# Optimization experiments

Hardware: AMD Instinct MI355X
Metric: run time of the kernel (lower is better)

## Reference

```python
import jax, jax.numpy as jnp
import numpy as np

# FP4 (E2M1) code table: nibble = [sign(1) | exp(2) | mantissa(1)]
# magnitudes for codes 0..7: 0, 0.5, 1, 1.5, 2, 3, 4, 6; codes 8..15 are negated.
_MAG = np.array([0.0, 0.5, 1.0, 1.5, 2.0, 3.0, 4.0, 6.0], dtype=np.float32)
FP4_LUT = jnp.asarray(np.concatenate([_MAG, -_MAG]))  # [16]

BLOCK = 16  # scale-factor block size along in_features


def setup_inputs() -> dict:
    key = jax.random.key(0)
    k0, k1, k2, k3, k4 = jax.random.split(key, 5)
    M, K, N = 32, 8192, 8192  # tokens, in_features, out_features
    inp = jax.random.normal(k0, (M, K), dtype=jnp.float32)
    qweight = jax.random.randint(k1, (N, K // 2), 0, 256, dtype=jnp.int32)  # packed FP4 pairs
    scales = jax.random.uniform(k2, (N, K // BLOCK), dtype=jnp.float32)      # per-block scales
    amax = jax.random.uniform(k3, (1,), dtype=jnp.float32) + 0.5             # global scale
    bias = jax.random.normal(k4, (N,), dtype=jnp.float32)
    return {"input": inp, "qweight": qweight, "scales": scales, "amax": amax, "bias": bias}


def _dequantize(qweight, scales, amax):
    N = qweight.shape[0]
    low = qweight & 0xF            # first element of each pair
    high = (qweight >> 4) & 0xF    # second element
    nibbles = jnp.stack([low, high], axis=-1).reshape(N, -1)  # [N, K]
    vals = FP4_LUT[nibbles]                                   # [N, K] fp4 values
    # per-block scaling: block of BLOCK contiguous in-features shares one scale
    w = (vals.reshape(N, -1, BLOCK) * scales[..., None]).reshape(N, -1)
    return w * amax[0]


def reference(input, qweight, scales, amax, bias):
    weight = _dequantize(qweight, scales, amax)   # [N, K] full-precision weight
    return input @ weight.T + bias                # F.linear
```

## Files before the change

### kernel.cpp

```cpp
#include <hip/hip_runtime.h>
#include <hip/hip_bf16.h>

#define M_DIM 32
#define K_DIM 8192
#define N_DIM 8192
#define KS 16
#define KCH (K_DIM / KS)
#define CHK 128
#define NCHK (KCH / CHK)
#define STEPS (CHK / 32)
#define NPB 128
#define MAIN_BLOCKS ((N_DIM / NPB) * KS)

#define QW_ROWI4 (K_DIM / 8)
#define SC_ROW (K_DIM / 16)

#define QROW 17
#define AROW 136
#define SROW 9

typedef _Float16 half8   __attribute__((ext_vector_type(8)));
typedef _Float16 half4_t __attribute__((ext_vector_type(4)));
typedef float    floatx4 __attribute__((ext_vector_type(4)));

__device__ __forceinline__ uint32_t dec2(uint32_t b) {
  uint32_t c0 = b & 0xFu, c1 = (b >> 4) & 0xFu;
  uint32_t m0 = c0 & 7u, m1 = c1 & 7u;
  uint32_t t0 = min(28u * m0, m0 + 28u);
  uint32_t t1 = min(28u * m1, m1 + 28u);
  return (t0 << 9) | ((c0 & 8u) << 12)
       | (t1 << 25) | ((c1 & 8u) << 28);
}

__device__ __forceinline__ half8 decode8p(uint32_t q, _Float16 s) {
  union { uint32_t u[4]; half8 h; } w;
  w.u[0] = dec2(q & 0xFFu);
  w.u[1] = dec2((q >> 8) & 0xFFu);
  w.u[2] = dec2((q >> 16) & 0xFFu);
  w.u[3] = dec2((q >> 24) & 0xFFu);
  half8 sv = {s, s, s, s, s, s, s, s};
  return w.h * sv;
}

__global__ void convertA_kernel(const floatx4* __restrict__ in4,
                                half4_t* __restrict__ out4) {
  int idx = blockIdx.x * blockDim.x + threadIdx.x;
  floatx4 f = in4[idx];
  half4_t h;
  h[0] = (_Float16)f[0]; h[1] = (_Float16)f[1];
  h[2] = (_Float16)f[2]; h[3] = (_Float16)f[3];
  out4[idx] = h;
}

__global__ void reduce_kernel(const floatx4* __restrict__ part,
                              const floatx4* __restrict__ bias4,
                              floatx4* __restrict__ out4) {
  int idx = blockIdx.x * blockDim.x + threadIdx.x;
  floatx4 acc = bias4[idx & (N_DIM / 4 - 1)];
#pragma unroll
  for (int s = 0; s < KS; ++s)
    acc += part[(size_t)s * (M_DIM * N_DIM / 4) + idx];
  out4[idx] = acc;
}

template <bool F16A>
__global__ __launch_bounds__(256, 4) void fp4_linear_kernel(
    const void*  __restrict__ Av,
    const int4*  __restrict__ qw4,
    const float* __restrict__ scales,
    const float* __restrict__ amaxp,
    float*       __restrict__ part)
{
  __shared__ uint32_t Qs[NPB * QROW];
  __shared__ _Float16 As[M_DIM * AROW];
  __shared__ float    Ss[NPB * SROW];

  const int t    = threadIdx.x;
  const int lane = t & 63;
  const int w    = t >> 6;
  const int ks   = blockIdx.x & (KS - 1);
  const int nb   = blockIdx.x >> 4;
  const int n0   = nb * NPB;
  const int kb   = ks * KCH;
  const float amax = amaxp[0];

  const int qr = t >> 4, qc = t & 15;
  const int4* qsrc = qw4 + (size_t)(n0 + qr) * QW_ROWI4 + ks * (KCH / 8) + qc;
  const int sr = t >> 1, sh = t & 1;
  const float* ssrc = scales + (size_t)(n0 + sr) * SC_ROW + ks * (KCH / 16) + sh * 4;
  const int ar16 = t >> 4, ac16 = t & 15;
  const _Float16* asrc16 =
      (const _Float16*)Av + (size_t)ar16 * K_DIM + kb + ac16 * 8;
  const int ar32 = t >> 5, ac32 = t & 31;
  const float* asrc32 = (const float*)Av + (size_t)ar32 * K_DIM + kb + ac32 * 4;

  int4    qreg[8];
  half8   areg16[2];
  floatx4 areg32[4];
  floatx4 sreg;

  {
#pragma unroll
    for (int j = 0; j < 8; ++j)
      qreg[j] = qsrc[(size_t)j * 16 * QW_ROWI4];
    if (F16A) {
#pragma unroll
      for (int j = 0; j < 2; ++j)
        areg16[j] = *(const half8*)(asrc16 + (size_t)j * 16 * K_DIM);
    } else {
#pragma unroll
      for (int j = 0; j < 4; ++j)
        areg32[j] = *(const floatx4*)(asrc32 + (size_t)j * 8 * K_DIM);
    }
    sreg = *(const floatx4*)ssrc;
  }

  const int row  = lane & 15;
  const int quad = lane >> 4;
  const int nloc = w * 32;
  const uint32_t* qAp = &Qs[(nloc + row) * QROW];
  const uint32_t* qBp = &Qs[(nloc + 16 + row) * QROW];
  const _Float16* a0p = &As[row * AROW];
  const _Float16* a1p = &As[(row + 16) * AROW];
  const float*    sAp = &Ss[(nloc + row) * SROW];
  const float*    sBp = &Ss[(nloc + 16 + row) * SROW];

  floatx4 acc00 = {0.f, 0.f, 0.f, 0.f};
  floatx4 acc01 = {0.f, 0.f, 0.f, 0.f};
  floatx4 acc10 = {0.f, 0.f, 0.f, 0.f};
  floatx4 acc11 = {0.f, 0.f, 0.f, 0.f};

  for (int c = 0; c < NCHK; ++c) {
    if (c) __syncthreads();

#pragma unroll
    for (int j = 0; j < 8; ++j) {
      uint32_t pk = ((uint32_t)qreg[j].x & 0xFFu)
                  | (((uint32_t)qreg[j].y & 0xFFu) << 8)
                  | (((uint32_t)qreg[j].z & 0xFFu) << 16)
                  | (((uint32_t)qreg[j].w & 0xFFu) << 24);
      Qs[(j * 16 + qr) * QROW + qc] = pk;
    }
    if (F16A) {
#pragma unroll
      for (int j = 0; j < 2; ++j)
        *(half8*)&As[(j * 16 + ar16) * AROW + ac16 * 8] = areg16[j];
    } else {
#pragma unroll
      for (int j = 0; j < 4; ++j) {
        floatx4 f = areg32[j];
        half4_t h;
        h[0] = (_Float16)f[0]; h[1] = (_Float16)f[1];
        h[2] = (_Float16)f[2]; h[3] = (_Float16)f[3];
        *(half4_t*)&As[(j * 8 + ar32) * AROW + ac32 * 4] = h;
      }
    }
    {
      float* sd = &Ss[sr * SROW + sh * 4];
      sd[0] = sreg[0] * amax; sd[1] = sreg[1] * amax;
      sd[2] = sreg[2] * amax; sd[3] = sreg[3] * amax;
    }
    __syncthreads();

    if (c + 1 < NCHK) {
      const int co = c + 1;
#pragma unroll
      for (int j = 0; j < 8; ++j)
        qreg[j] = qsrc[(size_t)j * 16 * QW_ROWI4 + co * (CHK / 8)];
      if (F16A) {
#pragma unroll
        for (int j = 0; j < 2; ++j)
          areg16[j] = *(const half8*)(asrc16 + (size_t)j * 16 * K_DIM + co * CHK);
      } else {
#pragma unroll
        for (int j = 0; j < 4; ++j)
          areg32[j] = *(const floatx4*)(asrc32 + (size_t)j * 8 * K_DIM + co * CHK);
      }
      sreg = *(const floatx4*)(ssrc + co * (CHK / 16));
    }

#pragma unroll
    for (int it = 0; it < STEPS; ++it) {
      const uint32_t qA = qAp[it * 4 + quad];
      const uint32_t qB = qBp[it * 4 + quad];
      const _Float16 sA = (_Float16)sAp[it * 2 + (quad >> 1)];
      const _Float16 sB = (_Float16)sBp[it * 2 + (quad >> 1)];
      half8 bA = decode8p(qA, sA);
      half8 bB = decode8p(qB, sB);
      half8 a0 = *(const half8*)(a0p + it * 32 + quad * 8);
      half8 a1 = *(const half8*)(a1p + it * 32 + quad * 8);
      acc00 = __builtin_amdgcn_mfma_f32_16x16x32_f16(a0, bA, acc00, 0, 0, 0);
      acc01 = __builtin_amdgcn_mfma_f32_16x16x32_f16(a0, bB, acc01, 0, 0, 0);
      acc10 = __builtin_amdgcn_mfma_f32_16x16x32_f16(a1, bA, acc10, 0, 0, 0);
      acc11 = __builtin_amdgcn_mfma_f32_16x16x32_f16(a1, bB, acc11, 0, 0, 0);
    }
  }

  float* pb = part + (size_t)ks * (M_DIM * N_DIM);
#pragma unroll
  for (int r = 0; r < 4; ++r) {
    const int m = quad * 4 + r;
    float* o0 = pb + (size_t)m * N_DIM + n0 + nloc;
    float* o1 = pb + (size_t)(m + 16) * N_DIM + n0 + nloc;
    o0[row]      = acc00[r];
    o0[16 + row] = acc01[r];
    o1[row]      = acc10[r];
    o1[16 + row] = acc11[r];
  }
}

extern "C" void kernel_launch(void* const* d_in, const int* in_sizes, int n_in,
                              void* d_out, int out_size, void* d_ws, size_t ws_size,
                              hipStream_t stream) {
  const float* inp    = (const float*)d_in[0];
  const int4*  qw4    = (const int4*)d_in[1];
  const float* scales = (const float*)d_in[2];
  const float* amaxp  = (const float*)d_in[3];
  const float* bias   = (const float*)d_in[4];
  float* out = (float*)d_out;

  const size_t part_bytes = (size_t)KS * M_DIM * N_DIM * sizeof(float);
  const size_t a16_bytes  = (size_t)M_DIM * K_DIM * sizeof(_Float16);
  float* partp = (float*)d_ws;

  if (ws_size >= part_bytes + a16_bytes) {
    _Float16* Af16 = (_Float16*)((char*)d_ws + part_bytes);
    convertA_kernel<<<M_DIM * K_DIM / 4 / 256, 256, 0, stream>>>(
        (const floatx4*)inp, (half4_t*)Af16);
    fp4_linear_kernel<true><<<MAIN_BLOCKS, 256, 0, stream>>>(
        Af16, qw4, scales, amaxp, partp);
  } else {
    fp4_linear_kernel<false><<<MAIN_BLOCKS, 256, 0, stream>>>(
        inp, qw4, scales, amaxp, partp);
  }
  reduce_kernel<<<M_DIM * N_DIM / 4 / 256, 256, 0, stream>>>(
      (const floatx4*)partp, (const floatx4*)bias, (floatx4*)out);
}
```

Baseline: 219.3 us.

## Repack FP4 weights into tile-contiguous layout before the main GEMM kernel

Adds a pre-pass kernel that compresses the int32-per-byte weight array into packed bytes arranged contiguously per block tile and k-chunk. The main kernel then loads each tile with two coalesced 16-byte loads per thread and stores them with vector LDS writes, instead of eight strided int4 loads plus packing. The fallback path is rewritten to use atomic accumulation into a bias-initialised output. The repack runs on every call and reads the full weight array, so it adds an extra pass over global memory.

Result: slower. 245.8 us (+12.1%).

```diff
diff --git a/kernel.cpp b/kernel.cpp
--- a/kernel.cpp
+++ b/kernel.cpp
@@ -10,14 +10,17 @@
 #define NCHK (KCH / CHK)
 #define STEPS (CHK / 32)
 #define NPB 128
-#define MAIN_BLOCKS ((N_DIM / NPB) * KS)
+#define NBLK (N_DIM / NPB)
+#define MAIN_BLOCKS (NBLK * KS)
 
 #define QW_ROWI4 (K_DIM / 8)
 #define SC_ROW (K_DIM / 16)
 
-#define QROW 17
+#define QROW 20
 #define AROW 136
 #define SROW 9
+
+#define QP_TILE_U4 512
 
 typedef _Float16 half8   __attribute__((ext_vector_type(8)));
 typedef _Float16 half4_t __attribute__((ext_vector_type(4)));
@@ -42,6 +45,27 @@
   return w.h * sv;
 }
 
+__device__ __forceinline__ uint32_t pack4(int4 v) {
+  return ((uint32_t)v.x & 0xFFu) | (((uint32_t)v.y & 0xFFu) << 8)
+       | (((uint32_t)v.z & 0xFFu) << 16) | (((uint32_t)v.w & 0xFFu) << 24);
+}
+
+__global__ __launch_bounds__(256) void repack_kernel(
+    const int4* __restrict__ qw4, uint4* __restrict__ qp) {
+  const int g  = blockIdx.x * 256 + threadIdx.x;
+  const int u  = g & 511;
+  const int c  = (g >> 9) & 3;
+  const int ks = (g >> 11) & 15;
+  const int nb = g >> 15;
+  const int r  = u >> 2, c4 = u & 3;
+  const int4* src = qw4 + (size_t)(nb * NPB + r) * QW_ROWI4
+                  + ks * (KCH / 8) + c * (CHK / 8) + c4 * 4;
+  int4 a = src[0], b = src[1], cc = src[2], d = src[3];
+  uint4 o;
+  o.x = pack4(a); o.y = pack4(b); o.z = pack4(cc); o.w = pack4(d);
+  qp[g] = o;
+}
+
 __global__ void convertA_kernel(const floatx4* __restrict__ in4,
                                 half4_t* __restrict__ out4) {
   int idx = blockIdx.x * blockDim.x + threadIdx.x;
@@ -63,13 +87,18 @@
   out4[idx] = acc;
 }
 
-template <bool F16A>
-__global__ __launch_bounds__(256, 4) void fp4_linear_kernel(
-    const void*  __restrict__ Av,
-    const int4*  __restrict__ qw4,
-    const float* __restrict__ scales,
-    const float* __restrict__ amaxp,
-    float*       __restrict__ part)
+__global__ void init_out_kernel(floatx4* __restrict__ out4,
+                                const floatx4* __restrict__ bias4) {
+  int idx = blockIdx.x * blockDim.x + threadIdx.x;
+  out4[idx] = bias4[idx & (N_DIM / 4 - 1)];
+}
+
+__global__ __launch_bounds__(256, 4) void fp4_linear_packed(
+    const _Float16* __restrict__ Af16,
+    const uint4*    __restrict__ qp,
+    const float*    __restrict__ scales,
+    const float*    __restrict__ amaxp,
+    float*          __restrict__ part)
 {
   __shared__ uint32_t Qs[NPB * QROW];
   __shared__ _Float16 As[M_DIM * AROW];
@@ -84,36 +113,21 @@
   const int kb   = ks * KCH;
   const float amax = amaxp[0];
 
-  const int qr = t >> 4, qc = t & 15;
-  const int4* qsrc = qw4 + (size_t)(n0 + qr) * QW_ROWI4 + ks * (KCH / 8) + qc;
+  const uint4* qtile = qp + (size_t)((nb * 16 + ks) * 4) * QP_TILE_U4;
+  const int ar = t >> 4, ac = t & 15;
+  const _Float16* asrc = Af16 + (size_t)ar * K_DIM + kb + ac * 8;
   const int sr = t >> 1, sh = t & 1;
   const float* ssrc = scales + (size_t)(n0 + sr) * SC_ROW + ks * (KCH / 16) + sh * 4;
-  const int ar16 = t >> 4, ac16 = t & 15;
-  const _Float16* asrc16 =
-      (const _Float16*)Av + (size_t)ar16 * K_DIM + kb + ac16 * 8;
-  const int ar32 = t >> 5, ac32 = t & 31;
-  const float* asrc32 = (const float*)Av + (size_t)ar32 * K_DIM + kb + ac32 * 4;
-
-  int4    qreg[8];
-  half8   areg16[2];
-  floatx4 areg32[4];
+
+  uint4   qreg[2];
+  half8   areg[2];
   floatx4 sreg;
 
-  {
-#pragma unroll
-    for (int j = 0; j < 8; ++j)
-      qreg[j] = qsrc[(size_t)j * 16 * QW_ROWI4];
-    if (F16A) {
-#pragma unroll
-      for (int j = 0; j < 2; ++j)
-        areg16[j] = *(const half8*)(asrc16 + (size_t)j * 16 * K_DIM);
-    } else {
-#pragma unroll
-      for (int j = 0; j < 4; ++j)
-        areg32[j] = *(const floatx4*)(asrc32 + (size_t)j * 8 * K_DIM);
-    }
-    sreg = *(const floatx4*)ssrc;
-  }
+  qreg[0] = qtile[t];
+  qreg[1] = qtile[256 + t];
+  areg[0] = *(const half8*)asrc;
+  areg[1] = *(const half8*)(asrc + (size_t)16 * K_DIM);
+  sreg = *(const floatx4*)ssrc;
 
   const int row  = lane & 15;
   const int quad = lane >> 4;
@@ -134,26 +148,11 @@
     if (c) __syncthreads();
 
 #pragma unroll
-    for (int j = 0; j < 8; ++j) {
-      uint32_t pk = ((uint32_t)qreg[j].x & 0xFFu)
-                  | (((uint32_t)qreg[j].y & 0xFFu) << 8)
-                  | (((uint32_t)qreg[j].z & 0xFFu) << 16)
-                  | (((uint32_t)qreg[j].w & 0xFFu) << 24);
-      Qs[(j * 16 + qr) * QROW + qc] = pk;
-    }
-    if (F16A) {
-#pragma unroll
-      for (int j = 0; j < 2; ++j)
-        *(half8*)&As[(j * 16 + ar16) * AROW + ac16 * 8] = areg16[j];
-    } else {
-#pragma unroll
-      for (int j = 0; j < 4; ++j) {
-        floatx4 f = areg32[j];
-        half4_t h;
-        h[0] = (_Float16)f[0]; h[1] = (_Float16)f[1];
-        h[2] = (_Float16)f[2]; h[3] = (_Float16)f[3];
-        *(half4_t*)&As[(j * 8 + ar32) * AROW + ac32 * 4] = h;
-      }
+    for (int j = 0; j < 2; ++j) {
+      const int u = j * 256 + t;
+      const int r = u >> 2, c4 = u & 3;
+      *(uint4*)&Qs[r * QROW + c4 * 4] = qreg[j];
+      *(half8*)&As[(j * 16 + ar) * AROW + ac * 8] = areg[j];
     }
     {
       float* sd = &Ss[sr * SROW + sh * 4];
@@ -163,20 +162,12 @@
     __syncthreads();
 
     if (c + 1 < NCHK) {
-      const int co = c + 1;
-#pragma unroll
-      for (int j = 0; j < 8; ++j)
-        qreg[j] = qsrc[(size_t)j * 16 * QW_ROWI4 + co * (CHK / 8)];
-      if (F16A) {
-#pragma unroll
-        for (int j = 0; j < 2; ++j)
-          areg16[j] = *(const half8*)(asrc16 + (size_t)j * 16 * K_DIM + co * CHK);
-      } else {
-#pragma unroll
-        for (int j = 0; j < 4; ++j)
-          areg32[j] = *(const floatx4*)(asrc32 + (size_t)j * 8 * K_DIM + co * CHK);
-      }
-      sreg = *(const floatx4*)(ssrc + co * (CHK / 16));
+      const int c1 = c + 1;
+      qreg[0] = qtile[c1 * QP_TILE_U4 + t];
+      qreg[1] = qtile[c1 * QP_TILE_U4 + 256 + t];
+      areg[0] = *(const half8*)(asrc + c1 * CHK);
+      areg[1] = *(const half8*)(asrc + (size_t)16 * K_DIM + c1 * CHK);
+      sreg = *(const floatx4*)(ssrc + c1 * (CHK / 16));
     }
 
 #pragma unroll
@@ -209,6 +200,50 @@
   }
 }
 
+__global__ __launch_bounds__(256, 4) void fp4_linear_fallback(
+    const float* __restrict__ inp, const int4* __restrict__ qw4,
+    const float* __restrict__ scales, const float* __restrict__ amaxp,
+    float* __restrict__ out) {
+  const int t = threadIdx.x, lane = t & 63, w = t >> 6;
+  const int ks = blockIdx.x & (KS - 1), nb = blockIdx.x >> 4;
+  const int n0 = nb * NPB, kb = ks * KCH;
+  const float amax = amaxp[0];
+  const int row = lane & 15, quad = lane >> 4, nloc = w * 32;
+  const int nA = n0 + nloc + row, nB = nA + 16;
+  const int4* qrowA = qw4 + (size_t)nA * QW_ROWI4;
+  const int4* qrowB = qw4 + (size_t)nB * QW_ROWI4;
+  const float* srowA = scales + (size_t)nA * SC_ROW;
+  const float* srowB = scales + (size_t)nB * SC_ROW;
+  floatx4 acc00 = {0,0,0,0}, acc01 = {0,0,0,0}, acc10 = {0,0,0,0}, acc11 = {0,0,0,0};
+  for (int k0 = kb; k0 < kb + KCH; k0 += 32) {
+    const int kq = k0 + quad * 8;
+    int4 qA = qrowA[kq >> 3], qB = qrowB[kq >> 3];
+    _Float16 sA = (_Float16)(srowA[kq >> 4] * amax);
+    _Float16 sB = (_Float16)(srowB[kq >> 4] * amax);
+    half8 bA = decode8p(pack4(qA), sA);
+    half8 bB = decode8p(pack4(qB), sB);
+    half8 a0, a1;
+    const float* ap0 = inp + (size_t)row * K_DIM + kq;
+    const float* ap1 = ap0 + (size_t)16 * K_DIM;
+#pragma unroll
+    for (int i = 0; i < 8; ++i) { a0[i] = (_Float16)ap0[i]; a1[i] = (_Float16)ap1[i]; }
+    acc00 = __builtin_amdgcn_mfma_f32_16x16x32_f16(a0, bA, acc00, 0, 0, 0);
+    acc01 = __builtin_amdgcn_mfma_f32_16x16x32_f16(a0, bB, acc01, 0, 0, 0);
+    acc10 = __builtin_amdgcn_mfma_f32_16x16x32_f16(a1, bA, acc10, 0, 0, 0);
+    acc11 = __builtin_amdgcn_mfma_f32_16x16x32_f16(a1, bB, acc11, 0, 0, 0);
+  }
+#pragma unroll
+  for (int r = 0; r < 4; ++r) {
+    const int m = quad * 4 + r;
+    float* o0 = out + (size_t)m * N_DIM + n0 + nloc;
+    float* o1 = out + (size_t)(m + 16) * N_DIM + n0 + nloc;
+    unsafeAtomicAdd(o0 + row,      acc00[r]);
+    unsafeAtomicAdd(o0 + 16 + row, acc01[r]);
+    unsafeAtomicAdd(o1 + row,      acc10[r]);
+    unsafeAtomicAdd(o1 + 16 + row, acc11[r]);
+  }
+}
+
 extern "C" void kernel_launch(void* const* d_in, const int* in_sizes, int n_in,
                               void* d_out, int out_size, void* d_ws, size_t ws_size,
                               hipStream_t stream) {
@@ -221,18 +256,23 @@
 
   const size_t part_bytes = (size_t)KS * M_DIM * N_DIM * sizeof(float);
   const size_t a16_bytes  = (size_t)M_DIM * K_DIM * sizeof(_Float16);
-  float* partp = (float*)d_ws;
-
-  if (ws_size >= part_bytes + a16_bytes) {
-    _Float16* Af16 = (_Float16*)((char*)d_ws + part_bytes);
+  const size_t qp_bytes   = (size_t)N_DIM * (K_DIM / 8) * 4;
+
+  if (ws_size >= part_bytes + a16_bytes + qp_bytes) {
+    float*    partp = (float*)d_ws;
+    _Float16* Af16  = (_Float16*)((char*)d_ws + part_bytes);
+    uint4*    qp    = (uint4*)((char*)d_ws + part_bytes + a16_bytes);
+    repack_kernel<<<8192, 256, 0, stream>>>(qw4, qp);
     convertA_kernel<<<M_DIM * K_DIM / 4 / 256, 256, 0, stream>>>(
         (const floatx4*)inp, (half4_t*)Af16);
-    fp4_linear_kernel<true><<<MAIN_BLOCKS, 256, 0, stream>>>(
-        Af16, qw4, scales, amaxp, partp);
+    fp4_linear_packed<<<MAIN_BLOCKS, 256, 0, stream>>>(
+        Af16, qp, scales, amaxp, partp);
+    reduce_kernel<<<M_DIM * N_DIM / 4 / 256, 256, 0, stream>>>(
+        (const floatx4*)partp, (const floatx4*)bias, (floatx4*)out);
   } else {
-    fp4_linear_kernel<false><<<MAIN_BLOCKS, 256, 0, stream>>>(
-        inp, qw4, scales, amaxp, partp);
-  }
-  reduce_kernel<<<M_DIM * N_DIM / 4 / 256, 256, 0, stream>>>(
-      (const floatx4*)partp, (const floatx4*)bias, (floatx4*)out);
-}
+    init_out_kernel<<<M_DIM * N_DIM / 4 / 256, 256, 0, stream>>>(
+        (floatx4*)out, (const floatx4*)bias);
+    fp4_linear_fallback<<<MAIN_BLOCKS, 256, 0, stream>>>(
+        inp, qw4, scales, amaxp, out);
+  }
+}
```
